# Kernel tuning notes

Hardware: AMD Instinct MI355X
Metric: run time of the kernel (lower is better)

The kernel has to match this reference:

```python
import jax, jax.numpy as jnp
import numpy as np

S = 3072      # total packed tokens
D = 1536      # hidden_size
H = 12        # num_heads
HD = D // H   # head_dim = 128
NSEQ = 4      # number of packed sequences (images)


def rotate_half(x):
    x1 = x[..., : x.shape[-1] // 2]
    x2 = x[..., x.shape[-1] // 2 :]
    return jnp.concatenate((-x2, x1), axis=-1)


def setup_inputs() -> dict:
    key = jax.random.key(0)
    k1, k2, k3 = jax.random.split(key, 3)
    hidden_states = jax.random.normal(k1, (S, D), jnp.float32)
    # 4 equal-length packed sequences
    cu_seqlens = (jnp.arange(NSEQ + 1, dtype=jnp.int32) * (S // NSEQ))
    # RoPE cos/sin per token, period within each packed sequence
    pos = (jnp.arange(S) % (S // NSEQ)).astype(jnp.float32)
    inv_freq = 1.0 / (10000.0 ** (jnp.arange(0, HD // 2, dtype=jnp.float32) / (HD // 2)))
    freqs = pos[:, None] * inv_freq[None, :]          # [S, HD//2]
    emb = jnp.concatenate([freqs, freqs], axis=-1)    # [S, HD]
    cos, sin = jnp.cos(emb), jnp.sin(emb)
    qkv_w = jax.random.normal(k2, (3 * D, D), jnp.float32) * (D ** -0.5)
    qkv_b = jnp.zeros((3 * D,), jnp.float32)
    proj_w = jax.random.normal(k3, (D, D), jnp.float32) * (D ** -0.5)
    return {
        "hidden_states": hidden_states,
        "cos": cos,
        "sin": sin,
        "qkv_w": qkv_w,
        "qkv_b": qkv_b,
        "proj_w": proj_w,
        "cu_seqlens": cu_seqlens,
    }


def reference(hidden_states, cos, sin, qkv_w, qkv_b, proj_w, cu_seqlens):
    s_len, dim = hidden_states.shape
    # fused QKV projection -> [S, 3, H, HD]
    qkv = (hidden_states @ qkv_w.T + qkv_b).reshape(s_len, 3, H, HD)
    q, k, v = qkv[:, 0], qkv[:, 1], qkv[:, 2]         # each [S, H, HD]
    # inline RoPE (fp32, broadcast over heads)
    c = cos[:, None, :].astype(jnp.float32)
    s = sin[:, None, :].astype(jnp.float32)
    qf, kf = q.astype(jnp.float32), k.astype(jnp.float32)
    q = (qf * c + rotate_half(qf) * s).astype(q.dtype)
    k = (kf * c + rotate_half(kf) * s).astype(k.dtype)
    # block-diagonal (varlen) mask from cu_seqlens
    seg = jnp.searchsorted(cu_seqlens, jnp.arange(s_len), side="right")  # [S]
    same_seq = seg[:, None] == seg[None, :]                              # [S, S]
    bias = jnp.where(same_seq, 0.0, -jnp.inf).astype(jnp.float32)
    scaling = HD ** -0.5
    # scores [H, S, S]
    scores = jnp.einsum("shd,thd->hst", q, k) * scaling + bias[None]
    probs = jax.nn.softmax(scores.astype(jnp.float32), axis=-1).astype(q.dtype)
    attn = jnp.einsum("hst,thd->shd", probs, v).reshape(s_len, dim)
    return attn @ proj_w.T
```

## Files before the change

kernel.cpp:

```cpp
#include <hip/hip_runtime.h>
#include <stdint.h>

#define S_LEN 3072
#define DIM   1536
#define NH    12
#define HD    128
#define QKV_N 4608

typedef unsigned short u16;
typedef __bf16 bf16x8 __attribute__((ext_vector_type(8)));
typedef float  f32x4  __attribute__((ext_vector_type(4)));
typedef u16    u16x8  __attribute__((ext_vector_type(8)));
typedef u16    u16x4  __attribute__((ext_vector_type(4)));

#define AS1 __attribute__((address_space(1)))
#define AS3 __attribute__((address_space(3)))
#define GLL16(g, l) __builtin_amdgcn_global_load_lds((AS1 void*)(g), (AS3 void*)(l), 16, 0, 0)

__device__ __forceinline__ u16 f2bf(float f) {
  unsigned u = __float_as_uint(f);
  u = (u + 0x7fffu + ((u >> 16) & 1u)) >> 16;
  return (u16)u;
}
__device__ __forceinline__ float bf2f(u16 b) {
  return __uint_as_float(((unsigned)b) << 16);
}

__global__ __launch_bounds__(256) void cvt_bf16_3(const float* __restrict__ in0, u16* __restrict__ out0, int n0,
                                                  const float* __restrict__ in1, u16* __restrict__ out1, int n1,
                                                  const float* __restrict__ in2, u16* __restrict__ out2, int n2) {
  int total = n0 + n1 + n2;
  int stride = gridDim.x * blockDim.x;
  for (int i = blockIdx.x * blockDim.x + threadIdx.x; i < total; i += stride) {
    const float* src; u16* dst; int j;
    if (i < n0)           { src = in0; dst = out0; j = i; }
    else if (i < n0 + n1) { src = in1; dst = out1; j = i - n0; }
    else                  { src = in2; dst = out2; j = i - n0 - n1; }
    float4 v = ((const float4*)src)[j];
    ushort4 o;
    o.x = f2bf(v.x); o.y = f2bf(v.y); o.z = f2bf(v.z); o.w = f2bf(v.w);
    ((ushort4*)dst)[j] = o;
  }
}

__device__ __forceinline__ bf16x8 frag2(const u16* region, int row, int ch) {
  int L = row >> 1;
  int slot = ((ch + ((row & 1) << 2)) ^ L) & 7;
  return *(const bf16x8*)(region + L * 64 + slot * 8);
}

__global__ __launch_bounds__(512, 2) void gemm_bt_256(const u16* __restrict__ A,
                                                      const u16* __restrict__ B,
                                                      const float* __restrict__ bias,
                                                      u16* __restrict__ Cout,
                                                      int M, int N, int K) {
  __shared__ __attribute__((aligned(16))) u16 lds[8 * 8192];

  const int t = threadIdx.x;
  const int l = t & 63;
  const int w = t >> 6;
  const int wm = w >> 2;
  const int wn = w & 3;
  const int lr = l & 15;
  const int lc = l >> 4;

  const int nbx = N >> 8;
  const int nwg = gridDim.x;
  const int q = nwg >> 3, r = nwg & 7;
  const int xcd = blockIdx.x & 7, rest = blockIdx.x >> 3;
  const int wgid = (xcd < r ? xcd * (q + 1) : r * (q + 1) + (xcd - r) * q) + rest;
  const int m0 = (wgid / nbx) * 256;
  const int n0 = (wgid % nbx) * 256;

  const int nk = K >> 6;

  f32x4 acc[8][4];
  #pragma unroll
  for (int i = 0; i < 8; ++i)
    #pragma unroll
    for (int j = 0; j < 4; ++j) acc[i][j] = f32x4{0.f, 0.f, 0.f, 0.f};

  auto stage_half = [&](int buf, int ks, int ab, int kt) {
    const u16* base = ab ? B : A;
    const int x0 = ab ? n0 : m0;
    u16* dst = lds + (((buf << 2) | (ks << 1) | ab) * 8192);
    #pragma unroll
    for (int i = 0; i < 2; ++i) {
      int C = t + i * 512;
      int L = C >> 3, s = C & 7;
      int u = s ^ (L & 7);
      int row = 2 * L + (u >> 2), ch = u & 3;
      const u16* src = base + (size_t)(x0 + row) * K + kt * 64 + ks * 32 + ch * 8;
      GLL16(src, dst + C * 8);
    }
  };

  stage_half(0, 0, 0, 0); stage_half(0, 0, 1, 0);
  stage_half(0, 1, 0, 0); stage_half(0, 1, 1, 0);
  if (nk > 1) { stage_half(1, 0, 0, 1); stage_half(1, 0, 1, 1); }
  asm volatile("s_waitcnt vmcnt(4)" ::: "memory");
  __builtin_amdgcn_s_barrier();

  for (int kt = 0; kt < nk; ++kt) {
    const int buf = kt & 1, nbuf = buf ^ 1;
    const bool st1 = (kt + 1 < nk);
    const bool st2 = (kt + 2 < nk);

    const u16* A0 = lds + (((buf << 2) | 0) * 8192);
    const u16* B0 = lds + (((buf << 2) | 1) * 8192);
    const u16* A1 = lds + (((buf << 2) | 2) * 8192);
    const u16* B1 = lds + (((buf << 2) | 3) * 8192);

    bf16x8 bfrag[4], afr[4];

    #pragma unroll
    for (int ni = 0; ni < 4; ++ni) bfrag[ni] = frag2(B0, wn * 64 + ni * 16 + lr, lc);
    #pragma unroll
    for (int mi = 0; mi < 4; ++mi) afr[mi] = frag2(A0, wm * 128 + mi * 16 + lr, lc);
    if (st1) stage_half(nbuf, 1, 0, kt + 1);
    __builtin_amdgcn_s_barrier();
    __builtin_amdgcn_s_setprio(1);
    #pragma unroll
    for (int mi = 0; mi < 4; ++mi)
      #pragma unroll
      for (int ni = 0; ni < 4; ++ni)
        acc[mi][ni] = __builtin_amdgcn_mfma_f32_16x16x32_bf16(afr[mi], bfrag[ni],
                                                              acc[mi][ni], 0, 0, 0);
    __builtin_amdgcn_s_setprio(0);
    __builtin_amdgcn_s_barrier();

    #pragma unroll
    for (int mi = 0; mi < 4; ++mi) afr[mi] = frag2(A0, wm * 128 + 64 + mi * 16 + lr, lc);
    if (st1) stage_half(nbuf, 1, 1, kt + 1);
    __builtin_amdgcn_s_barrier();
    __builtin_amdgcn_s_setprio(1);
    #pragma unroll
    for (int mi = 0; mi < 4; ++mi)
      #pragma unroll
      for (int ni = 0; ni < 4; ++ni)
        acc[4 + mi][ni] = __builtin_amdgcn_mfma_f32_16x16x32_bf16(afr[mi], bfrag[ni],
                                                                  acc[4 + mi][ni], 0, 0, 0);
    __builtin_amdgcn_s_setprio(0);
    __builtin_amdgcn_s_barrier();

    #pragma unroll
    for (int ni = 0; ni < 4; ++ni) bfrag[ni] = frag2(B1, wn * 64 + ni * 16 + lr, lc);
    #pragma unroll
    for (int mi = 0; mi < 4; ++mi) afr[mi] = frag2(A1, wm * 128 + mi * 16 + lr, lc);
    if (st2) stage_half(buf, 0, 0, kt + 2);
    __builtin_amdgcn_s_barrier();
    __builtin_amdgcn_s_setprio(1);
    #pragma unroll
    for (int mi = 0; mi < 4; ++mi)
      #pragma unroll
      for (int ni = 0; ni < 4; ++ni)
        acc[mi][ni] = __builtin_amdgcn_mfma_f32_16x16x32_bf16(afr[mi], bfrag[ni],
                                                              acc[mi][ni], 0, 0, 0);
    __builtin_amdgcn_s_setprio(0);
    __builtin_amdgcn_s_barrier();

    #pragma unroll
    for (int mi = 0; mi < 4; ++mi) afr[mi] = frag2(A1, wm * 128 + 64 + mi * 16 + lr, lc);
    if (st2) {
      stage_half(buf, 0, 1, kt + 2);
      asm volatile("s_waitcnt vmcnt(4)" ::: "memory");
    } else if (st1) {
      asm volatile("s_waitcnt vmcnt(0)" ::: "memory");
    }
    __builtin_amdgcn_s_barrier();
    __builtin_amdgcn_s_setprio(1);
    #pragma unroll
    for (int mi = 0; mi < 4; ++mi)
      #pragma unroll
      for (int ni = 0; ni < 4; ++ni)
        acc[4 + mi][ni] = __builtin_amdgcn_mfma_f32_16x16x32_bf16(afr[mi], bfrag[ni],
                                                                  acc[4 + mi][ni], 0, 0, 0);
    __builtin_amdgcn_s_setprio(0);
    __builtin_amdgcn_s_barrier();
  }

  {
    float bv[4];
    #pragma unroll
    for (int ni = 0; ni < 4; ++ni)
      bv[ni] = bias ? bias[n0 + wn * 64 + ni * 16 + lr] : 0.f;
    #pragma unroll
    for (int mi = 0; mi < 8; ++mi) {
      int row = wm * 128 + mi * 16 + lc * 4;
      #pragma unroll
      for (int ni = 0; ni < 4; ++ni) {
        int scol = (wn * 64 + ni * 16 + lr) ^ (lc << 4);
        #pragma unroll
        for (int rr = 0; rr < 4; ++rr)
          lds[(row + rr) * 256 + scol] = f2bf(acc[mi][ni][rr] + bv[ni]);
      }
    }
    __syncthreads();
    #pragma unroll
    for (int i = 0; i < 16; ++i) {
      int id = i * 512 + t;
      int row = id >> 5, c16 = id & 31;
      int s = (row >> 2) & 3;
      u16x8 v = *(const u16x8*)(lds + row * 256 + ((c16 * 8) ^ (s << 4)));
      *(u16x8*)(Cout + (size_t)(m0 + row) * N + n0 + c16 * 8) = v;
    }
  }
}

__device__ __forceinline__ bf16x8 lds_frag(const u16* base, int row, int ch) {
  return *(const bf16x8*)(base + row * 64 + ((ch ^ row) & 7) * 8);
}

template <bool BIAS, bool OUTF32>
__global__ __launch_bounds__(256) void gemm_bt(const u16* __restrict__ A,
                                               const u16* __restrict__ B,
                                               const float* __restrict__ bias,
                                               void* __restrict__ Cout,
                                               int M, int N, int K) {
  __shared__ u16 Asm[128 * 64];
  __shared__ u16 Bsm[128 * 64];
  const int t = threadIdx.x;
  const int l = t & 63;
  const int w = t >> 6;
  const int wm = w >> 1, wn = w & 1;
  const int m0 = blockIdx.y * 128, n0 = blockIdx.x * 128;

  f32x4 acc[4][4];
  #pragma unroll
  for (int i = 0; i < 4; ++i)
    #pragma unroll
    for (int j = 0; j < 4; ++j) acc[i][j] = f32x4{0.f, 0.f, 0.f, 0.f};

  for (int k0 = 0; k0 < K; k0 += 64) {
    __syncthreads();
    #pragma unroll
    for (int r4 = 0; r4 < 4; ++r4) {
      int C = t + r4 * 256;
      int row = C >> 3, ch = C & 7;
      int sch = (ch ^ row) & 7;
      GLL16(A + (size_t)(m0 + row) * K + k0 + sch * 8, Asm + (size_t)C * 8);
      GLL16(B + (size_t)(n0 + row) * K + k0 + sch * 8, Bsm + (size_t)C * 8);
    }
    __syncthreads();
    #pragma unroll
    for (int ks = 0; ks < 2; ++ks) {
      bf16x8 af[4], bfr[4];
      #pragma unroll
      for (int mi = 0; mi < 4; ++mi)
        af[mi] = lds_frag(Asm, wm * 64 + mi * 16 + (l & 15), ks * 4 + (l >> 4));
      #pragma unroll
      for (int ni = 0; ni < 4; ++ni)
        bfr[ni] = lds_frag(Bsm, wn * 64 + ni * 16 + (l & 15), ks * 4 + (l >> 4));
      #pragma unroll
      for (int mi = 0; mi < 4; ++mi)
        #pragma unroll
        for (int ni = 0; ni < 4; ++ni)
          acc[mi][ni] = __builtin_amdgcn_mfma_f32_16x16x32_bf16(af[mi], bfr[ni],
                                                                acc[mi][ni], 0, 0, 0);
    }
  }

  #pragma unroll
  for (int ni = 0; ni < 4; ++ni) {
    int col = n0 + wn * 64 + ni * 16 + (l & 15);
    float bv = 0.f;
    if (BIAS) bv = bias[col];
    #pragma unroll
    for (int mi = 0; mi < 4; ++mi) {
      int rbase = m0 + wm * 64 + mi * 16 + ((l >> 4) << 2);
      #pragma unroll
      for (int rr = 0; rr < 4; ++rr) {
        float v = acc[mi][ni][rr] + bv;
        if (OUTF32)
          ((float*)Cout)[(size_t)(rbase + rr) * N + col] = v;
        else
          ((u16*)Cout)[(size_t)(rbase + rr) * N + col] = f2bf(v);
      }
    }
  }
}

__global__ __launch_bounds__(256) void rope_pack(const u16* __restrict__ QKV,
                                                 const float* __restrict__ cosb,
                                                 const float* __restrict__ sinb,
                                                 u16* __restrict__ Qp,
                                                 u16* __restrict__ Kp,
                                                 u16* __restrict__ Vt) {
  __shared__ u16 vtile[64][128];
  const int t = threadIdx.x;
  const int s0 = blockIdx.x * 64;
  const int h = blockIdx.y;

  const int srow = s0 + (t >> 2);
  const int d0 = (t & 3) * 16;
  const u16* qkvrow = QKV + (size_t)srow * QKV_N + h * HD;
  const float qscale = 0.08838834764831845f * 1.4426950408889634f;

  float cl[16], chh[16], sl[16], shh[16];
  #pragma unroll
  for (int g = 0; g < 4; ++g) {
    *(float4*)(cl + 4 * g)  = *(const float4*)(cosb + srow * HD + d0 + 4 * g);
    *(float4*)(chh + 4 * g) = *(const float4*)(cosb + srow * HD + d0 + 64 + 4 * g);
    *(float4*)(sl + 4 * g)  = *(const float4*)(sinb + srow * HD + d0 + 4 * g);
    *(float4*)(shh + 4 * g) = *(const float4*)(sinb + srow * HD + d0 + 64 + 4 * g);
  }

  #pragma unroll
  for (int which = 0; which < 2; ++which) {
    const u16* src = qkvrow + which * DIM;
    u16* dst = (which ? Kp : Qp) + ((size_t)h * S_LEN + srow) * HD;
    const float sc = which ? 1.f : qscale;
    u16x8 xl0 = *(const u16x8*)(src + d0);
    u16x8 xl1 = *(const u16x8*)(src + d0 + 8);
    u16x8 xh0 = *(const u16x8*)(src + d0 + 64);
    u16x8 xh1 = *(const u16x8*)(src + d0 + 72);
    u16x8 o0, o1, o2, o3;
    #pragma unroll
    for (int j = 0; j < 8; ++j) {
      float xlo = bf2f(xl0[j]), xhi = bf2f(xh0[j]);
      o0[j] = f2bf((xlo * cl[j] - xhi * sl[j]) * sc);
      o2[j] = f2bf((xhi * chh[j] + xlo * shh[j]) * sc);
      float xlo2 = bf2f(xl1[j]), xhi2 = bf2f(xh1[j]);
      o1[j] = f2bf((xlo2 * cl[j + 8] - xhi2 * sl[j + 8]) * sc);
      o3[j] = f2bf((xhi2 * chh[j + 8] + xlo2 * shh[j + 8]) * sc);
    }
    *(u16x8*)(dst + d0)      = o0;
    *(u16x8*)(dst + d0 + 8)  = o1;
    *(u16x8*)(dst + d0 + 64) = o2;
    *(u16x8*)(dst + d0 + 72) = o3;
  }

  #pragma unroll
  for (int r4 = 0; r4 < 4; ++r4) {
    int C = t + r4 * 256;
    int row = C >> 4, ch = C & 15;
    *(uint4*)(&vtile[row][ch * 8]) =
        *(const uint4*)(QKV + (size_t)(s0 + row) * QKV_N + 2 * DIM + h * HD + ch * 8);
  }
  __syncthreads();
  const int d = t >> 1;
  const int sc0 = (t & 1) * 32;
  u16* vdst = Vt + ((size_t)h * HD + d) * S_LEN + s0 + sc0;
  #pragma unroll
  for (int j = 0; j < 32; j += 8) {
    u16x8 v;
    #pragma unroll
    for (int e = 0; e < 8; ++e) v[e] = vtile[sc0 + j + e][d];
    *(u16x8*)(vdst + j) = v;
  }
}

__global__ __launch_bounds__(256) void attn_fwd(const u16* __restrict__ Qp,
                                                const u16* __restrict__ Kp,
                                                const u16* __restrict__ Vt,
                                                const int* __restrict__ cu,
                                                u16* __restrict__ Obf) {
  __shared__ u16 K_lds[64 * 128];
  __shared__ u16 VT_lds[128 * 64];
  __shared__ u16 P_lds[4][16 * 76];

  const int t = threadIdx.x;
  const int l = t & 63;
  const int w = t >> 6;
  const int lr = l & 15;
  const int lq = l >> 4;
  const int q0 = blockIdx.x * 64;
  const int h = blockIdx.y;

  int cs = 0, ce = S_LEN;
  #pragma unroll
  for (int b = 0; b < 4; ++b) {
    int lo = cu[b], hi = cu[b + 1];
    if (q0 >= lo && q0 < hi) { cs = lo; ce = hi; }
  }

  const int qrow = q0 + w * 16 + lr;
  bf16x8 qf[4];
  const u16* qptr = Qp + ((size_t)h * S_LEN + qrow) * HD + lq * 8;
  #pragma unroll
  for (int ks = 0; ks < 4; ++ks) qf[ks] = *(const bf16x8*)(qptr + ks * 32);

  f32x4 acc_o[8];
  #pragma unroll
  for (int i = 0; i < 8; ++i) acc_o[i] = f32x4{0.f, 0.f, 0.f, 0.f};
  float m_run = -1e30f, l_run = 0.f;

  for (int kv0 = cs; kv0 < ce; kv0 += 64) {
    __syncthreads();
    {
      const u16* kbase = Kp + ((size_t)h * S_LEN + kv0) * HD;
      #pragma unroll
      for (int r4 = 0; r4 < 4; ++r4) {
        int C = t + r4 * 256;
        int row = C >> 4, ch = C & 15;
        int sch = (ch & 8) | ((ch ^ row) & 7);
        GLL16(kbase + row * HD + sch * 8, K_lds + (size_t)C * 8);
      }
      const u16* vbase = Vt + (size_t)h * HD * S_LEN + kv0;
      #pragma unroll
      for (int r4 = 0; r4 < 4; ++r4) {
        int C = t + r4 * 256;
        int row = C >> 3, ch = C & 7;
        int sch = (ch ^ row) & 7;
        GLL16(vbase + (size_t)row * S_LEN + sch * 8, VT_lds + (size_t)C * 8);
      }
    }
    __syncthreads();

    f32x4 s_acc[4];
    __builtin_amdgcn_s_setprio(1);
    #pragma unroll
    for (int nf = 0; nf < 4; ++nf) {
      s_acc[nf] = f32x4{0.f, 0.f, 0.f, 0.f};
      int krow = nf * 16 + lr;
      #pragma unroll
      for (int ks = 0; ks < 4; ++ks) {
        int ch = ks * 4 + lq;
        int sch = (ch & 8) | ((ch ^ krow) & 7);
        bf16x8 kf = *(const bf16x8*)(K_lds + krow * 128 + sch * 8);
        s_acc[nf] = __builtin_amdgcn_mfma_f32_16x16x32_bf16(kf, qf[ks], s_acc[nf], 0, 0, 0);
      }
    }
    __builtin_amdgcn_s_setprio(0);

    float vmax = -1e30f;
    #pragma unroll
    for (int nf = 0; nf < 4; ++nf)
      #pragma unroll
      for (int r = 0; r < 4; ++r) vmax = fmaxf(vmax, s_acc[nf][r]);
    vmax = fmaxf(vmax, __shfl_xor(vmax, 16, 64));
    vmax = fmaxf(vmax, __shfl_xor(vmax, 32, 64));
    float mn = fmaxf(m_run, vmax);
    float alpha = __builtin_amdgcn_exp2f(m_run - mn);
    m_run = mn;
    float pv[4][4], sum = 0.f;
    #pragma unroll
    for (int nf = 0; nf < 4; ++nf)
      #pragma unroll
      for (int r = 0; r < 4; ++r) {
        float e = __builtin_amdgcn_exp2f(s_acc[nf][r] - mn);
        pv[nf][r] = e;
        sum += e;
      }
    sum += __shfl_xor(sum, 16, 64);
    sum += __shfl_xor(sum, 32, 64);
    l_run = l_run * alpha + sum;

    float alphaO[4];
    #pragma unroll
    for (int r = 0; r < 4; ++r) alphaO[r] = __shfl(alpha, lq * 20 + r, 64);
    #pragma unroll
    for (int onf = 0; onf < 8; ++onf)
      #pragma unroll
      for (int r = 0; r < 4; ++r) acc_o[onf][r] *= alphaO[r];

    u16* pl = P_lds[w];
    #pragma unroll
    for (int nf = 0; nf < 4; ++nf) {
      u16x4 pk;
      #pragma unroll
      for (int r = 0; r < 4; ++r) pk[r] = f2bf(pv[nf][r]);
      *(u16x4*)(pl + lr * 76 + nf * 16 + lq * 4) = pk;
    }

    __builtin_amdgcn_s_setprio(1);
    #pragma unroll
    for (int ks = 0; ks < 2; ++ks) {
      bf16x8 pa = *(const bf16x8*)(pl + lr * 76 + ks * 32 + lq * 8);
      #pragma unroll
      for (int onf = 0; onf < 8; ++onf) {
        int d = onf * 16 + lr;
        int ch = ks * 4 + lq;
        int sch = (ch ^ d) & 7;
        bf16x8 vf = *(const bf16x8*)(VT_lds + d * 64 + sch * 8);
        acc_o[onf] = __builtin_amdgcn_mfma_f32_16x16x32_bf16(pa, vf, acc_o[onf], 0, 0, 0);
      }
    }
    __builtin_amdgcn_s_setprio(0);
  }

  float invO[4];
  #pragma unroll
  for (int r = 0; r < 4; ++r) invO[r] = 1.f / __shfl(l_run, lq * 20 + r, 64);
  #pragma unroll
  for (int r = 0; r < 4; ++r) {
    int srow = q0 + w * 16 + (lq << 2) + r;
    u16* orow = Obf + (size_t)srow * DIM + h * HD + lr;
    #pragma unroll
    for (int onf = 0; onf < 8; ++onf) orow[onf * 16] = f2bf(acc_o[onf][r] * invO[r]);
  }
}

extern "C" void kernel_launch(void* const* d_in, const int* in_sizes, int n_in,
                              void* d_out, int out_size, void* d_ws, size_t ws_size,
                              hipStream_t stream) {
  const float* hidden = (const float*)d_in[0];
  const float* cosb   = (const float*)d_in[1];
  const float* sinb   = (const float*)d_in[2];
  const float* qkv_w  = (const float*)d_in[3];
  const float* qkv_b  = (const float*)d_in[4];
  const float* proj_w = (const float*)d_in[5];
  const int*   cu     = (const int*)d_in[6];

  u16* Hbf   = (u16*)d_ws;
  u16* Wqkv  = Hbf   + (size_t)S_LEN * DIM;
  u16* Wproj = Wqkv  + (size_t)QKV_N * DIM;
  u16* QKVbf = Wproj + (size_t)DIM * DIM;
  u16* Kp    = QKVbf + (size_t)S_LEN * QKV_N;
  u16* Vt    = Kp    + (size_t)NH * S_LEN * HD;
  u16* Qp    = Wqkv;
  u16* Abf   = Hbf;

  cvt_bf16_3<<<2048, 256, 0, stream>>>(hidden, Hbf, S_LEN * DIM / 4,
                                       qkv_w, Wqkv, QKV_N * DIM / 4,
                                       proj_w, Wproj, DIM * DIM / 4);

  gemm_bt_256<<<(S_LEN / 256) * (QKV_N / 256), 512, 0, stream>>>(
      Hbf, Wqkv, qkv_b, QKVbf, S_LEN, QKV_N, DIM);

  rope_pack<<<dim3(S_LEN / 64, NH), 256, 0, stream>>>(QKVbf, cosb, sinb, Qp, Kp, Vt);

  attn_fwd<<<dim3(S_LEN / 64, NH), 256, 0, stream>>>(Qp, Kp, Vt, cu, Abf);

  gemm_bt<false, true><<<dim3(DIM / 128, S_LEN / 128), 256, 0, stream>>>(
      Abf, Wproj, nullptr, d_out, S_LEN, DIM, DIM);
}
```

Before: 154.8 us.

## Restructure QKV GEMM to 128x256 tiles with B fragments loaded directly from global

Replaces the 256x256, 512-thread QKV GEMM with a 128x256, 256-thread kernel. Only the A tile is staged in LDS, while each wave loads its B (weight) fragments straight from global memory into registers and double-buffers them across k-halves. The pipeline drops from four barrier-separated phases per k-step to two, and LDS use shrinks, so more workgroups and a larger grid fit on the device. The cost is that weight reads now skip LDS, so each workgroup rereads B and global traffic for B goes up. Latency hiding for those register loads depends on the hand-written vmcnt waits.

Result: slower. 175.3 us (+13.3%).

```diff
diff --git a/kernel.cpp b/kernel.cpp
--- a/kernel.cpp
+++ b/kernel.cpp
@@ -43,35 +43,26 @@
   }
 }
 
-__device__ __forceinline__ bf16x8 frag2(const u16* region, int row, int ch) {
-  int L = row >> 1;
-  int slot = ((ch + ((row & 1) << 2)) ^ L) & 7;
-  return *(const bf16x8*)(region + L * 64 + slot * 8);
-}
-
-__global__ __launch_bounds__(512, 2) void gemm_bt_256(const u16* __restrict__ A,
-                                                      const u16* __restrict__ B,
-                                                      const float* __restrict__ bias,
-                                                      u16* __restrict__ Cout,
-                                                      int M, int N, int K) {
-  __shared__ __attribute__((aligned(16))) u16 lds[8 * 8192];
+__global__ __launch_bounds__(256, 2) void gemm_qkv(const u16* __restrict__ A,
+                                                   const u16* __restrict__ B,
+                                                   const float* __restrict__ bias,
+                                                   u16* __restrict__ Cout,
+                                                   int M, int N, int K) {
+  __shared__ __attribute__((aligned(16))) u16 lds[32768];
 
   const int t = threadIdx.x;
   const int l = t & 63;
   const int w = t >> 6;
-  const int wm = w >> 2;
-  const int wn = w & 3;
   const int lr = l & 15;
-  const int lc = l >> 4;
+  const int lq = l >> 4;
 
   const int nbx = N >> 8;
   const int nwg = gridDim.x;
   const int q = nwg >> 3, r = nwg & 7;
   const int xcd = blockIdx.x & 7, rest = blockIdx.x >> 3;
   const int wgid = (xcd < r ? xcd * (q + 1) : r * (q + 1) + (xcd - r) * q) + rest;
-  const int m0 = (wgid / nbx) * 256;
+  const int m0 = (wgid / nbx) * 128;
   const int n0 = (wgid % nbx) * 256;
-
   const int nk = K >> 6;
 
   f32x4 acc[8][4];
@@ -80,102 +71,74 @@
     #pragma unroll
     for (int j = 0; j < 4; ++j) acc[i][j] = f32x4{0.f, 0.f, 0.f, 0.f};
 
-  auto stage_half = [&](int buf, int ks, int ab, int kt) {
-    const u16* base = ab ? B : A;
-    const int x0 = ab ? n0 : m0;
-    u16* dst = lds + (((buf << 2) | (ks << 1) | ab) * 8192);
+  auto stageA = [&](int buf, int ks, int kt) {
+    u16* dst = lds + ((buf << 1) | ks) * 4096;
     #pragma unroll
     for (int i = 0; i < 2; ++i) {
-      int C = t + i * 512;
-      int L = C >> 3, s = C & 7;
-      int u = s ^ (L & 7);
-      int row = 2 * L + (u >> 2), ch = u & 3;
-      const u16* src = base + (size_t)(x0 + row) * K + kt * 64 + ks * 32 + ch * 8;
-      GLL16(src, dst + C * 8);
+      int C = t + i * 256;
+      int row = C >> 2, slot = C & 3;
+      int ch = slot ^ (row & 3);
+      GLL16(A + (size_t)(m0 + row) * K + kt * 64 + ks * 32 + ch * 8, dst + C * 8);
     }
   };
-
-  stage_half(0, 0, 0, 0); stage_half(0, 0, 1, 0);
-  stage_half(0, 1, 0, 0); stage_half(0, 1, 1, 0);
-  if (nk > 1) { stage_half(1, 0, 0, 1); stage_half(1, 0, 1, 1); }
-  asm volatile("s_waitcnt vmcnt(4)" ::: "memory");
+  auto loadB = [&](bf16x8* bf, int kt, int ks) {
+    #pragma unroll
+    for (int ni = 0; ni < 4; ++ni)
+      bf[ni] = *(const bf16x8*)(B + (size_t)(n0 + w * 64 + ni * 16 + lr) * K +
+                                kt * 64 + ks * 32 + lq * 8);
+  };
+  auto readA = [&](bf16x8* af, int buf, int ks) {
+    const u16* reg = lds + ((buf << 1) | ks) * 4096;
+    #pragma unroll
+    for (int mi = 0; mi < 8; ++mi) {
+      int row = mi * 16 + lr;
+      int slot = lq ^ (row & 3);
+      af[mi] = *(const bf16x8*)(reg + row * 32 + slot * 8);
+    }
+  };
+
+  bf16x8 bA[4], bB[4];
+  stageA(0, 0, 0);
+  stageA(0, 1, 0);
+  loadB(bA, 0, 0);
+  asm volatile("s_waitcnt vmcnt(6)" ::: "memory");
   __builtin_amdgcn_s_barrier();
 
   for (int kt = 0; kt < nk; ++kt) {
     const int buf = kt & 1, nbuf = buf ^ 1;
-    const bool st1 = (kt + 1 < nk);
-    const bool st2 = (kt + 2 < nk);
-
-    const u16* A0 = lds + (((buf << 2) | 0) * 8192);
-    const u16* B0 = lds + (((buf << 2) | 1) * 8192);
-    const u16* A1 = lds + (((buf << 2) | 2) * 8192);
-    const u16* B1 = lds + (((buf << 2) | 3) * 8192);
-
-    bf16x8 bfrag[4], afr[4];
-
-    #pragma unroll
-    for (int ni = 0; ni < 4; ++ni) bfrag[ni] = frag2(B0, wn * 64 + ni * 16 + lr, lc);
-    #pragma unroll
-    for (int mi = 0; mi < 4; ++mi) afr[mi] = frag2(A0, wm * 128 + mi * 16 + lr, lc);
-    if (st1) stage_half(nbuf, 1, 0, kt + 1);
+    const bool st = (kt + 1 < nk);
+
+    loadB(bB, kt, 1);
+    if (st) stageA(nbuf, 0, kt + 1);
+    {
+      bf16x8 af[8];
+      readA(af, buf, 0);
+      __builtin_amdgcn_s_setprio(1);
+      #pragma unroll
+      for (int mi = 0; mi < 8; ++mi)
+        #pragma unroll
+        for (int ni = 0; ni < 4; ++ni)
+          acc[mi][ni] = __builtin_amdgcn_mfma_f32_16x16x32_bf16(af[mi], bA[ni],
+                                                                acc[mi][ni], 0, 0, 0);
+      __builtin_amdgcn_s_setprio(0);
+    }
+    asm volatile("s_waitcnt vmcnt(4)" ::: "memory");
     __builtin_amdgcn_s_barrier();
-    __builtin_amdgcn_s_setprio(1);
-    #pragma unroll
-    for (int mi = 0; mi < 4; ++mi)
-      #pragma unroll
-      for (int ni = 0; ni < 4; ++ni)
-        acc[mi][ni] = __builtin_amdgcn_mfma_f32_16x16x32_bf16(afr[mi], bfrag[ni],
-                                                              acc[mi][ni], 0, 0, 0);
-    __builtin_amdgcn_s_setprio(0);
-    __builtin_amdgcn_s_barrier();
-
-    #pragma unroll
-    for (int mi = 0; mi < 4; ++mi) afr[mi] = frag2(A0, wm * 128 + 64 + mi * 16 + lr, lc);
-    if (st1) stage_half(nbuf, 1, 1, kt + 1);
-    __builtin_amdgcn_s_barrier();
-    __builtin_amdgcn_s_setprio(1);
-    #pragma unroll
-    for (int mi = 0; mi < 4; ++mi)
-      #pragma unroll
-      for (int ni = 0; ni < 4; ++ni)
-        acc[4 + mi][ni] = __builtin_amdgcn_mfma_f32_16x16x32_bf16(afr[mi], bfrag[ni],
-                                                                  acc[4 + mi][ni], 0, 0, 0);
-    __builtin_amdgcn_s_setprio(0);
-    __builtin_amdgcn_s_barrier();
-
-    #pragma unroll
-    for (int ni = 0; ni < 4; ++ni) bfrag[ni] = frag2(B1, wn * 64 + ni * 16 + lr, lc);
-    #pragma unroll
-    for (int mi = 0; mi < 4; ++mi) afr[mi] = frag2(A1, wm * 128 + mi * 16 + lr, lc);
-    if (st2) stage_half(buf, 0, 0, kt + 2);
-    __builtin_amdgcn_s_barrier();
-    __builtin_amdgcn_s_setprio(1);
-    #pragma unroll
-    for (int mi = 0; mi < 4; ++mi)
-      #pragma unroll
-      for (int ni = 0; ni < 4; ++ni)
-        acc[mi][ni] = __builtin_amdgcn_mfma_f32_16x16x32_bf16(afr[mi], bfrag[ni],
-                                                              acc[mi][ni], 0, 0, 0);
-    __builtin_amdgcn_s_setprio(0);
-    __builtin_amdgcn_s_barrier();
-
-    #pragma unroll
-    for (int mi = 0; mi < 4; ++mi) afr[mi] = frag2(A1, wm * 128 + 64 + mi * 16 + lr, lc);
-    if (st2) {
-      stage_half(buf, 0, 1, kt + 2);
-      asm volatile("s_waitcnt vmcnt(4)" ::: "memory");
-    } else if (st1) {
-      asm volatile("s_waitcnt vmcnt(0)" ::: "memory");
-    }
-    __builtin_amdgcn_s_barrier();
-    __builtin_amdgcn_s_setprio(1);
-    #pragma unroll
-    for (int mi = 0; mi < 4; ++mi)
-      #pragma unroll
-      for (int ni = 0; ni < 4; ++ni)
-        acc[4 + mi][ni] = __builtin_amdgcn_mfma_f32_16x16x32_bf16(afr[mi], bfrag[ni],
-                                                                  acc[4 + mi][ni], 0, 0, 0);
-    __builtin_amdgcn_s_setprio(0);
+
+    if (st) { loadB(bA, kt + 1, 0); stageA(nbuf, 1, kt + 1); }
+    {
+      bf16x8 af[8];
+      readA(af, buf, 1);
+      __builtin_amdgcn_s_setprio(1);
+      #pragma unroll
+      for (int mi = 0; mi < 8; ++mi)
+        #pragma unroll
+        for (int ni = 0; ni < 4; ++ni)
+          acc[mi][ni] = __builtin_amdgcn_mfma_f32_16x16x32_bf16(af[mi], bB[ni],
+                                                                acc[mi][ni], 0, 0, 0);
+      __builtin_amdgcn_s_setprio(0);
+    }
+    asm volatile("s_waitcnt vmcnt(6)" ::: "memory");
     __builtin_amdgcn_s_barrier();
   }
 
@@ -183,13 +146,13 @@
     float bv[4];
     #pragma unroll
     for (int ni = 0; ni < 4; ++ni)
-      bv[ni] = bias ? bias[n0 + wn * 64 + ni * 16 + lr] : 0.f;
+      bv[ni] = bias ? bias[n0 + w * 64 + ni * 16 + lr] : 0.f;
     #pragma unroll
     for (int mi = 0; mi < 8; ++mi) {
-      int row = wm * 128 + mi * 16 + lc * 4;
+      int row = mi * 16 + lq * 4;
       #pragma unroll
       for (int ni = 0; ni < 4; ++ni) {
-        int scol = (wn * 64 + ni * 16 + lr) ^ (lc << 4);
+        int scol = (w * 64 + ni * 16 + lr) ^ (lq << 4);
         #pragma unroll
         for (int rr = 0; rr < 4; ++rr)
           lds[(row + rr) * 256 + scol] = f2bf(acc[mi][ni][rr] + bv[ni]);
@@ -198,7 +161,7 @@
     __syncthreads();
     #pragma unroll
     for (int i = 0; i < 16; ++i) {
-      int id = i * 512 + t;
+      int id = i * 256 + t;
       int row = id >> 5, c16 = id & 31;
       int s = (row >> 2) & 3;
       u16x8 v = *(const u16x8*)(lds + row * 256 + ((c16 * 8) ^ (s << 4)));
@@ -515,7 +478,7 @@
                                        qkv_w, Wqkv, QKV_N * DIM / 4,
                                        proj_w, Wproj, DIM * DIM / 4);
 
-  gemm_bt_256<<<(S_LEN / 256) * (QKV_N / 256), 512, 0, stream>>>(
+  gemm_qkv<<<(S_LEN / 128) * (QKV_N / 256), 256, 0, stream>>>(
       Hbf, Wqkv, qkv_b, QKVbf, S_LEN, QKV_N, DIM);
 
   rope_pack<<<dim3(S_LEN / 64, NH), 256, 0, stream>>>(QKVbf, cosb, sinb, Qp, Kp, Vt);
```

## Fuse RoPE, Q/K packing and V transpose into QKV GEMM epilogue

Applied to the files above, without the earlier changes.

The QKV GEMM epilogue now applies RoPE and the query scale while writing Q and K in head-major layout, and writes V transposed straight from the LDS tile. This removes the separate rope_pack kernel and the round trip of the full QKV intermediate through global memory. The LDS swizzle is widened so the rotate-half partner and column-wise V reads stay conflict-light. The epilogue gains cos/sin loads and strided LDS reads, and Qp no longer aliases the weight buffer.

New measurement: 150.9 us. -2.5%, faster.

```diff
diff --git a/kernel.cpp b/kernel.cpp
--- a/kernel.cpp
+++ b/kernel.cpp
@@ -43,17 +43,15 @@
   }
 }
 
-__device__ __forceinline__ bf16x8 frag2(const u16* region, int row, int ch) {
-  int L = row >> 1;
-  int slot = ((ch + ((row & 1) << 2)) ^ L) & 7;
-  return *(const bf16x8*)(region + L * 64 + slot * 8);
-}
-
-__global__ __launch_bounds__(512, 2) void gemm_bt_256(const u16* __restrict__ A,
-                                                      const u16* __restrict__ B,
-                                                      const float* __restrict__ bias,
-                                                      u16* __restrict__ Cout,
-                                                      int M, int N, int K) {
+__global__ __launch_bounds__(512, 2) void gemm_qkvf(const u16* __restrict__ A,
+                                                    const u16* __restrict__ B,
+                                                    const float* __restrict__ bias,
+                                                    const float* __restrict__ cosb,
+                                                    const float* __restrict__ sinb,
+                                                    u16* __restrict__ Qp,
+                                                    u16* __restrict__ Kp,
+                                                    u16* __restrict__ Vt,
+                                                    int M, int N, int K) {
   __shared__ __attribute__((aligned(16))) u16 lds[8 * 8192];
 
   const int t = threadIdx.x;
@@ -80,6 +78,11 @@
     #pragma unroll
     for (int j = 0; j < 4; ++j) acc[i][j] = f32x4{0.f, 0.f, 0.f, 0.f};
 
+  auto frag2 = [&](const u16* region, int row, int ch) {
+    int L = row >> 1;
+    int slot = ((ch + ((row & 1) << 2)) ^ L) & 7;
+    return *(const bf16x8*)(region + L * 64 + slot * 8);
+  };
   auto stage_half = [&](int buf, int ks, int ab, int kt) {
     const u16* base = ab ? B : A;
     const int x0 = ab ? n0 : m0;
@@ -179,30 +182,69 @@
     __builtin_amdgcn_s_barrier();
   }
 
+  const int sec = n0 / DIM;
+  const int h0 = (n0 % DIM) >> 7;
+
   {
     float bv[4];
     #pragma unroll
     for (int ni = 0; ni < 4; ++ni)
-      bv[ni] = bias ? bias[n0 + wn * 64 + ni * 16 + lr] : 0.f;
+      bv[ni] = bias[n0 + wn * 64 + ni * 16 + lr];
     #pragma unroll
     for (int mi = 0; mi < 8; ++mi) {
-      int row = wm * 128 + mi * 16 + lc * 4;
+      int rbase = wm * 128 + mi * 16 + lc * 4;
+      int s4 = (mi * 4 + lc) & 15;
       #pragma unroll
       for (int ni = 0; ni < 4; ++ni) {
-        int scol = (wn * 64 + ni * 16 + lr) ^ (lc << 4);
+        int scol = (wn * 64 + ni * 16 + lr) ^ (s4 << 4);
         #pragma unroll
         for (int rr = 0; rr < 4; ++rr)
-          lds[(row + rr) * 256 + scol] = f2bf(acc[mi][ni][rr] + bv[ni]);
-      }
-    }
-    __syncthreads();
+          lds[(rbase + rr) * 256 + scol] = f2bf(acc[mi][ni][rr] + bv[ni]);
+      }
+    }
+  }
+  __syncthreads();
+
+  if (sec < 2) {
+    u16* dst = sec ? Kp : Qp;
+    const float sc = sec ? 1.f : (0.08838834764831845f * 1.4426950408889634f);
     #pragma unroll
     for (int i = 0; i < 16; ++i) {
       int id = i * 512 + t;
       int row = id >> 5, c16 = id & 31;
-      int s = (row >> 2) & 3;
-      u16x8 v = *(const u16x8*)(lds + row * 256 + ((c16 * 8) ^ (s << 4)));
-      *(u16x8*)(Cout + (size_t)(m0 + row) * N + n0 + c16 * 8) = v;
+      int srow = m0 + row;
+      int s4 = (row >> 2) & 15;
+      int c8 = c16 * 8;
+      u16x8 x  = *(const u16x8*)(lds + row * 256 + (c8 ^ (s4 << 4)));
+      u16x8 xp = *(const u16x8*)(lds + row * 256 + ((c8 ^ 64) ^ (s4 << 4)));
+      int h = h0 + (c8 >> 7);
+      int d = c8 & 127;
+      float cs[8], sn[8];
+      *(float4*)(cs)     = *(const float4*)(cosb + (size_t)srow * HD + d);
+      *(float4*)(cs + 4) = *(const float4*)(cosb + (size_t)srow * HD + d + 4);
+      *(float4*)(sn)     = *(const float4*)(sinb + (size_t)srow * HD + d);
+      *(float4*)(sn + 4) = *(const float4*)(sinb + (size_t)srow * HD + d + 4);
+      const float sg = (d & 64) ? 1.f : -1.f;
+      u16x8 o;
+      #pragma unroll
+      for (int j = 0; j < 8; ++j)
+        o[j] = f2bf((bf2f(x[j]) * cs[j] + sg * bf2f(xp[j]) * sn[j]) * sc);
+      *(u16x8*)(dst + ((size_t)h * S_LEN + srow) * HD + d) = o;
+    }
+  } else {
+    #pragma unroll
+    for (int i = 0; i < 16; ++i) {
+      int id = i * 512 + t;
+      int col = id >> 5, sch = id & 31;
+      int h = h0 + (col >> 7), d = col & 127;
+      u16x8 v;
+      #pragma unroll
+      for (int e = 0; e < 8; ++e) {
+        int row = sch * 8 + e;
+        int s4 = (row >> 2) & 15;
+        v[e] = lds[row * 256 + (col ^ (s4 << 4))];
+      }
+      *(u16x8*)(Vt + ((size_t)h * HD + d) * S_LEN + m0 + sch * 8) = v;
     }
   }
 }
@@ -280,76 +322,6 @@
   }
 }
 
-__global__ __launch_bounds__(256) void rope_pack(const u16* __restrict__ QKV,
-                                                 const float* __restrict__ cosb,
-                                                 const float* __restrict__ sinb,
-                                                 u16* __restrict__ Qp,
-                                                 u16* __restrict__ Kp,
-                                                 u16* __restrict__ Vt) {
-  __shared__ u16 vtile[64][128];
-  const int t = threadIdx.x;
-  const int s0 = blockIdx.x * 64;
-  const int h = blockIdx.y;
-
-  const int srow = s0 + (t >> 2);
-  const int d0 = (t & 3) * 16;
-  const u16* qkvrow = QKV + (size_t)srow * QKV_N + h * HD;
-  const float qscale = 0.08838834764831845f * 1.4426950408889634f;
-
-  float cl[16], chh[16], sl[16], shh[16];
-  #pragma unroll
-  for (int g = 0; g < 4; ++g) {
-    *(float4*)(cl + 4 * g)  = *(const float4*)(cosb + srow * HD + d0 + 4 * g);
-    *(float4*)(chh + 4 * g) = *(const float4*)(cosb + srow * HD + d0 + 64 + 4 * g);
-    *(float4*)(sl + 4 * g)  = *(const float4*)(sinb + srow * HD + d0 + 4 * g);
-    *(float4*)(shh + 4 * g) = *(const float4*)(sinb + srow * HD + d0 + 64 + 4 * g);
-  }
-
-  #pragma unroll
-  for (int which = 0; which < 2; ++which) {
-    const u16* src = qkvrow + which * DIM;
-    u16* dst = (which ? Kp : Qp) + ((size_t)h * S_LEN + srow) * HD;
-    const float sc = which ? 1.f : qscale;
-    u16x8 xl0 = *(const u16x8*)(src + d0);
-    u16x8 xl1 = *(const u16x8*)(src + d0 + 8);
-    u16x8 xh0 = *(const u16x8*)(src + d0 + 64);
-    u16x8 xh1 = *(const u16x8*)(src + d0 + 72);
-    u16x8 o0, o1, o2, o3;
-    #pragma unroll
-    for (int j = 0; j < 8; ++j) {
-      float xlo = bf2f(xl0[j]), xhi = bf2f(xh0[j]);
-      o0[j] = f2bf((xlo * cl[j] - xhi * sl[j]) * sc);
-      o2[j] = f2bf((xhi * chh[j] + xlo * shh[j]) * sc);
-      float xlo2 = bf2f(xl1[j]), xhi2 = bf2f(xh1[j]);
-      o1[j] = f2bf((xlo2 * cl[j + 8] - xhi2 * sl[j + 8]) * sc);
-      o3[j] = f2bf((xhi2 * chh[j + 8] + xlo2 * shh[j + 8]) * sc);
-    }
-    *(u16x8*)(dst + d0)      = o0;
-    *(u16x8*)(dst + d0 + 8)  = o1;
-    *(u16x8*)(dst + d0 + 64) = o2;
-    *(u16x8*)(dst + d0 + 72) = o3;
-  }
-
-  #pragma unroll
-  for (int r4 = 0; r4 < 4; ++r4) {
-    int C = t + r4 * 256;
-    int row = C >> 4, ch = C & 15;
-    *(uint4*)(&vtile[row][ch * 8]) =
-        *(const uint4*)(QKV + (size_t)(s0 + row) * QKV_N + 2 * DIM + h * HD + ch * 8);
-  }
-  __syncthreads();
-  const int d = t >> 1;
-  const int sc0 = (t & 1) * 32;
-  u16* vdst = Vt + ((size_t)h * HD + d) * S_LEN + s0 + sc0;
-  #pragma unroll
-  for (int j = 0; j < 32; j += 8) {
-    u16x8 v;
-    #pragma unroll
-    for (int e = 0; e < 8; ++e) v[e] = vtile[sc0 + j + e][d];
-    *(u16x8*)(vdst + j) = v;
-  }
-}
-
 __global__ __launch_bounds__(256) void attn_fwd(const u16* __restrict__ Qp,
                                                 const u16* __restrict__ Kp,
                                                 const u16* __restrict__ Vt,
@@ -505,20 +477,17 @@
   u16* Hbf   = (u16*)d_ws;
   u16* Wqkv  = Hbf   + (size_t)S_LEN * DIM;
   u16* Wproj = Wqkv  + (size_t)QKV_N * DIM;
-  u16* QKVbf = Wproj + (size_t)DIM * DIM;
-  u16* Kp    = QKVbf + (size_t)S_LEN * QKV_N;
+  u16* Qp    = Wproj + (size_t)DIM * DIM;
+  u16* Kp    = Qp    + (size_t)NH * S_LEN * HD;
   u16* Vt    = Kp    + (size_t)NH * S_LEN * HD;
-  u16* Qp    = Wqkv;
   u16* Abf   = Hbf;
 
   cvt_bf16_3<<<2048, 256, 0, stream>>>(hidden, Hbf, S_LEN * DIM / 4,
                                        qkv_w, Wqkv, QKV_N * DIM / 4,
                                        proj_w, Wproj, DIM * DIM / 4);
 
-  gemm_bt_256<<<(S_LEN / 256) * (QKV_N / 256), 512, 0, stream>>>(
-      Hbf, Wqkv, qkv_b, QKVbf, S_LEN, QKV_N, DIM);
-
-  rope_pack<<<dim3(S_LEN / 64, NH), 256, 0, stream>>>(QKVbf, cosb, sinb, Qp, Kp, Vt);
+  gemm_qkvf<<<(S_LEN / 256) * (QKV_N / 256), 512, 0, stream>>>(
+      Hbf, Wqkv, qkv_b, cosb, sinb, Qp, Kp, Vt, S_LEN, QKV_N, DIM);
 
   attn_fwd<<<dim3(S_LEN / 64, NH), 256, 0, stream>>>(Qp, Kp, Vt, cu, Abf);
 
```
